# Kernel tuning notes

Hardware: AMD Instinct MI355X
Metric: run time of the kernel (lower is better)

## Reference

```python
import jax, jax.numpy as jnp
import numpy as np

N = 50000      # nodes
E = 600000     # edges
D_IN = 5
D_H = 128
EPS = 1e-5     # BatchNorm1d default eps


def batch_norm(x, gamma, beta):
    # training-mode BN over the node dimension (biased variance)
    m = jnp.mean(x, axis=0)
    v = jnp.var(x, axis=0)
    return (x - m) * jax.lax.rsqrt(v + EPS) * gamma + beta


def gcn_conv(x, W, b, src, dst, w):
    # PyG GCNConv: linear transform, add self-loops (weight 1),
    # symmetric normalization D^-1/2 A D^-1/2, scatter-add to dst, + bias.
    x = x @ W                                   # [N, out]
    n = x.shape[0]
    loop = jnp.arange(n)
    src = jnp.concatenate([src, loop])
    dst = jnp.concatenate([dst, loop])
    w = jnp.concatenate([w, jnp.ones((n,), w.dtype)])
    deg = jax.ops.segment_sum(w, dst, num_segments=n)
    dis = jnp.where(deg > 0, jax.lax.rsqrt(jnp.maximum(deg, 1e-12)), 0.0)
    norm = dis[src] * w * dis[dst]              # [E+N]
    msgs = norm[:, None] * x[src]               # gather + scale
    return jax.ops.segment_sum(msgs, dst, num_segments=n) + b


def setup_inputs() -> dict:
    key = jax.random.key(0)
    ks = jax.random.split(key, 20)
    s_in = 1.0 / np.sqrt(D_IN)
    s_h = 1.0 / np.sqrt(D_H)
    return {
        "h": jax.random.normal(ks[0], (N, D_IN), jnp.float32),
        "edge_index": jax.random.randint(ks[1], (2, E), 0, N),
        "edge_weight": jax.random.uniform(ks[2], (E,), jnp.float32),
        "g0": 1.0 + 0.1 * jax.random.normal(ks[3], (D_IN,), jnp.float32),
        "be0": 0.1 * jax.random.normal(ks[4], (D_IN,), jnp.float32),
        "W1": jax.random.normal(ks[5], (D_IN, D_H), jnp.float32) * s_in,
        "b1": jax.random.normal(ks[6], (D_H,), jnp.float32) * s_in,
        "g1": 1.0 + 0.1 * jax.random.normal(ks[7], (D_H,), jnp.float32),
        "be1": 0.1 * jax.random.normal(ks[8], (D_H,), jnp.float32),
        "W2": jax.random.normal(ks[9], (D_H, D_H), jnp.float32) * s_h,
        "b2": jax.random.normal(ks[10], (D_H,), jnp.float32) * s_h,
        "g2": 1.0 + 0.1 * jax.random.normal(ks[11], (D_H,), jnp.float32),
        "be2": 0.1 * jax.random.normal(ks[12], (D_H,), jnp.float32),
        "Wmu": jax.random.normal(ks[13], (D_H, D_H), jnp.float32) * s_h,
        "bmu": jax.random.normal(ks[14], (D_H,), jnp.float32) * s_h,
        "Wls": jax.random.normal(ks[15], (D_H, D_H), jnp.float32) * s_h,
        "bls": jax.random.normal(ks[16], (D_H,), jnp.float32) * s_h,
    }


def reference(h, edge_index, edge_weight, g0, be0, W1, b1, g1, be1,
              W2, b2, g2, be2, Wmu, bmu, Wls, bls):
    src, dst = edge_index[0], edge_index[1]
    h = batch_norm(h, g0, be0)
    h = jax.nn.relu(batch_norm(gcn_conv(h, W1, b1, src, dst, edge_weight), g1, be1))
    # dropout p=0.1 treated as eval-mode (identity)
    h = jax.nn.relu(batch_norm(gcn_conv(h, W2, b2, src, dst, edge_weight), g2, be2))
    mu = h @ Wmu + bmu
    log_std = h @ Wls + bls
    return (mu, log_std)
```

## Files before the change

kernel.cpp:

```cpp
#include <hip/hip_runtime.h>

#define N_NODES 50000
#define N_EDGES 600000
#define D_IN 5
#define D_H 128
#define BN_EPS 1e-5f
#define SCAN_BLOCKS ((N_NODES + 255) / 256)
#define FIX_SCALE 16777216.0f
#define FIX_INV   (1.0f / 16777216.0f)

typedef __bf16 bf16x8 __attribute__((ext_vector_type(8)));
typedef float  f32x4  __attribute__((ext_vector_type(4)));

__device__ inline unsigned short f2bfb(float f) {
    unsigned u = __builtin_bit_cast(unsigned, f);
    unsigned r = u + 0x7fffu + ((u >> 16) & 1u);
    return (unsigned short)(r >> 16);
}
__device__ inline float bflo(unsigned u) { return __builtin_bit_cast(float, u << 16); }
__device__ inline float bfhi(unsigned u) { return __builtin_bit_cast(float, u & 0xffff0000u); }

__device__ inline void stage_b(const unsigned short* __restrict__ Bt,
                               uint4* __restrict__ lds, int t)
{
#pragma unroll
    for (int i = 0; i < 8; ++i) {
        int slot = i * 256 + t;
        int fid = slot >> 6;
        int l = slot & 63;
        int row = (fid >> 2) * 16 + (l & 15);
        int boff = ((l >> 4) * 16 + (fid & 3) * 64) >> 1;
        lds[slot] = *(const uint4*)(Bt + row * D_H + boff);
    }
}

__global__ __launch_bounds__(256) void k_wprep(const float* __restrict__ W2,
                                               const float* __restrict__ Wmu,
                                               const float* __restrict__ Wls,
                                               unsigned short* __restrict__ T2,
                                               unsigned short* __restrict__ Tmu,
                                               unsigned short* __restrict__ Tls)
{
    int mat = blockIdx.x >> 6;
    int idx = (blockIdx.x & 63) * 256 + threadIdx.x;
    const float* W = (mat == 0) ? W2 : (mat == 1) ? Wmu : Wls;
    unsigned short* T = (mat == 0) ? T2 : (mat == 1) ? Tmu : Tls;
    int k = idx >> 7, n = idx & 127;
    T[n * D_H + k] = f2bfb(W[idx]);
}

__global__ __launch_bounds__(256) void k_bn0_stats(const float* __restrict__ h,
                                                   float* __restrict__ stats)
{
    __shared__ float ss[D_IN], sq[D_IN];
    int t = threadIdx.x;
    if (t < D_IN) { ss[t] = 0.f; sq[t] = 0.f; }
    __syncthreads();
    int node = blockIdx.x * blockDim.x + t;
    float v[D_IN];
#pragma unroll
    for (int f = 0; f < D_IN; ++f)
        v[f] = (node < N_NODES) ? h[node * D_IN + f] : 0.f;
    int lane = t & 63;
#pragma unroll
    for (int f = 0; f < D_IN; ++f) {
        float s = v[f], q = v[f] * v[f];
        for (int off = 32; off > 0; off >>= 1) {
            s += __shfl_down(s, off);
            q += __shfl_down(q, off);
        }
        if (lane == 0) { atomicAdd(&ss[f], s); atomicAdd(&sq[f], q); }
    }
    __syncthreads();
    if (t < D_IN) {
        atomicAdd(&stats[t], ss[t]);
        atomicAdd(&stats[D_IN + t], sq[t]);
    }
}

__global__ __launch_bounds__(256) void k_deg_count(const int* __restrict__ dst,
                                                   const float* __restrict__ w,
                                                   unsigned long long* __restrict__ degcnt)
{
    int e = blockIdx.x * blockDim.x + threadIdx.x;
    if (e < N_EDGES) {
        int d = dst[e];
        unsigned long long fx = (unsigned long long)(w[e] * FIX_SCALE + 0.5f);
        atomicAdd(degcnt + d, (1ull << 40) | fx);
    }
}

__global__ __launch_bounds__(256) void k_scan1(const unsigned long long* __restrict__ degcnt,
                                               float* __restrict__ dis,
                                               int* __restrict__ blocksums)
{
    __shared__ int sm[256];
    int t = threadIdx.x;
    int i = blockIdx.x * 256 + t;
    int c = 0;
    if (i < N_NODES) {
        unsigned long long v = degcnt[i];
        c = (int)(v >> 40);
        float deg = (float)(v & ((1ull << 40) - 1)) * FIX_INV;
        dis[i] = rsqrtf(deg + 1.0f);
    }
    sm[t] = c;
    __syncthreads();
    for (int off = 128; off > 0; off >>= 1) {
        if (t < off) sm[t] += sm[t + off];
        __syncthreads();
    }
    if (t == 0) blocksums[blockIdx.x] = sm[0];
}

__global__ __launch_bounds__(256) void k_scan2(int* __restrict__ blocksums,
                                               int* __restrict__ rowptr)
{
    __shared__ int sm[256];
    int t = threadIdx.x;
    int c = (t < SCAN_BLOCKS) ? blocksums[t] : 0;
    sm[t] = c;
    __syncthreads();
    for (int off = 1; off < 256; off <<= 1) {
        int v = (t >= off) ? sm[t - off] : 0;
        __syncthreads();
        sm[t] += v;
        __syncthreads();
    }
    if (t < SCAN_BLOCKS) blocksums[t] = sm[t] - c;
    if (t == 255) rowptr[N_NODES] = sm[255];
}

__global__ __launch_bounds__(256) void k_scan3(const unsigned long long* __restrict__ degcnt,
                                               int* __restrict__ rowptr,
                                               int* __restrict__ cursor,
                                               const int* __restrict__ blocksums)
{
    __shared__ int sm[256];
    int t = threadIdx.x;
    int i = blockIdx.x * 256 + t;
    int c = (i < N_NODES) ? (int)(degcnt[i] >> 40) : 0;
    sm[t] = c;
    __syncthreads();
    for (int off = 1; off < 256; off <<= 1) {
        int v = (t >= off) ? sm[t - off] : 0;
        __syncthreads();
        sm[t] += v;
        __syncthreads();
    }
    if (i < N_NODES) {
        int pos = blocksums[blockIdx.x] + sm[t] - c;
        rowptr[i] = pos;
        cursor[i] = pos;
    }
}

__global__ __launch_bounds__(256) void k_fill(const int* __restrict__ src,
                                              const int* __restrict__ dst,
                                              const float* __restrict__ w,
                                              const float* __restrict__ dis,
                                              int* __restrict__ cursor,
                                              int2* __restrict__ csr)
{
    int e = blockIdx.x * blockDim.x + threadIdx.x;
    if (e < N_EDGES) {
        int s = src[e], d = dst[e];
        float nm = dis[s] * w[e] * dis[d];
        int pos = atomicAdd(cursor + d, 1);
        int2 pk;
        pk.x = s;
        pk.y = __builtin_bit_cast(int, nm);
        csr[pos] = pk;
    }
}

__global__ __launch_bounds__(256) void k_agg0(const float* __restrict__ h,
                                              const float* __restrict__ stats,
                                              const float* __restrict__ g0,
                                              const float* __restrict__ be0,
                                              const int* __restrict__ rowptr,
                                              const int2* __restrict__ csr,
                                              const float* __restrict__ dis,
                                              float* __restrict__ agg)
{
    int n = blockIdx.x * blockDim.x + threadIdx.x;
    if (n >= N_NODES) return;
    float sc[D_IN], sh[D_IN];
#pragma unroll
    for (int f = 0; f < D_IN; ++f) {
        float m = stats[f] * (1.0f / N_NODES);
        float var = stats[D_IN + f] * (1.0f / N_NODES) - m * m;
        sc[f] = rsqrtf(var + BN_EPS) * g0[f];
        sh[f] = be0[f] - m * sc[f];
    }
    float dn = dis[n];
    float sl = dn * dn;
    float acc[D_IN];
#pragma unroll
    for (int f = 0; f < D_IN; ++f)
        acc[f] = sl * (h[n * D_IN + f] * sc[f] + sh[f]);
    int e0 = rowptr[n], e1 = rowptr[n + 1];
    for (int e = e0; e < e1; ++e) {
        int2 pk = csr[e];
        int s = pk.x;
        float nm = __builtin_bit_cast(float, pk.y);
#pragma unroll
        for (int f = 0; f < D_IN; ++f)
            acc[f] += nm * (h[s * D_IN + f] * sc[f] + sh[f]);
    }
#pragma unroll
    for (int f = 0; f < D_IN; ++f)
        agg[n * D_IN + f] = acc[f];
}

__global__ __launch_bounds__(256) void k_l1(const float* __restrict__ agg,
                                            const float* __restrict__ W1,
                                            const float* __restrict__ b1,
                                            float* __restrict__ x,
                                            float* __restrict__ stats)
{
    __shared__ float sm_s[256], sm_q[256];
    int t = threadIdx.x;
    int idx0 = blockIdx.x * 256 + t;
    int f = idx0 & (D_H - 1);
    float w[D_IN];
#pragma unroll
    for (int k = 0; k < D_IN; ++k) w[k] = W1[k * D_H + f];
    float b = b1[f];
    float s = 0.f, q = 0.f;
    const int stride = 512 * 256;
    for (int idx = idx0; idx < N_NODES * D_H; idx += stride) {
        int n = idx >> 7;
        const float* a = agg + n * D_IN;
        float v = b;
#pragma unroll
        for (int k = 0; k < D_IN; ++k) v += w[k] * a[k];
        x[idx] = v;
        s += v;
        q += v * v;
    }
    sm_s[t] = s;
    sm_q[t] = q;
    __syncthreads();
    if (t < D_H) {
        atomicAdd(stats + t, sm_s[t] + sm_s[t + D_H]);
        atomicAdd(stats + D_H + t, sm_q[t] + sm_q[t + D_H]);
    }
}

__global__ __launch_bounds__(256) void k_bn_relu_f32_bf16(const float* __restrict__ x,
                                                          const float* __restrict__ stats,
                                                          const float* __restrict__ g,
                                                          const float* __restrict__ be,
                                                          unsigned short* __restrict__ y)
{
    int i4 = blockIdx.x * blockDim.x + threadIdx.x;
    if (i4 >= N_NODES * D_H / 4) return;
    int f0 = (i4 & 31) * 4;
    float4 s4 = *(const float4*)(stats + f0);
    float4 q4 = *(const float4*)(stats + D_H + f0);
    float4 g4 = *(const float4*)(g + f0);
    float4 b4 = *(const float4*)(be + f0);
    float4 v = *(const float4*)(x + (size_t)i4 * 4);
    const float inv = 1.0f / N_NODES;
    float m, var, sc, sh;
    float r0, r1, r2, r3;
    m = s4.x * inv; var = q4.x * inv - m * m; sc = rsqrtf(var + BN_EPS) * g4.x; sh = b4.x - m * sc;
    r0 = fmaxf(v.x * sc + sh, 0.f);
    m = s4.y * inv; var = q4.y * inv - m * m; sc = rsqrtf(var + BN_EPS) * g4.y; sh = b4.y - m * sc;
    r1 = fmaxf(v.y * sc + sh, 0.f);
    m = s4.z * inv; var = q4.z * inv - m * m; sc = rsqrtf(var + BN_EPS) * g4.z; sh = b4.z - m * sc;
    r2 = fmaxf(v.z * sc + sh, 0.f);
    m = s4.w * inv; var = q4.w * inv - m * m; sc = rsqrtf(var + BN_EPS) * g4.w; sh = b4.w - m * sc;
    r3 = fmaxf(v.w * sc + sh, 0.f);
    uint2 o;
    o.x = (unsigned)f2bfb(r0) | ((unsigned)f2bfb(r1) << 16);
    o.y = (unsigned)f2bfb(r2) | ((unsigned)f2bfb(r3) << 16);
    *(uint2*)(y + (size_t)i4 * 4) = o;
}

__global__ __launch_bounds__(256) void k_bn_relu_bf16_bf16(const unsigned short* __restrict__ x,
                                                           const float* __restrict__ stats,
                                                           const float* __restrict__ g,
                                                           const float* __restrict__ be,
                                                           unsigned short* __restrict__ y)
{
    int i4 = blockIdx.x * blockDim.x + threadIdx.x;
    if (i4 >= N_NODES * D_H / 4) return;
    int f0 = (i4 & 31) * 4;
    float4 s4 = *(const float4*)(stats + f0);
    float4 q4 = *(const float4*)(stats + D_H + f0);
    float4 g4 = *(const float4*)(g + f0);
    float4 b4 = *(const float4*)(be + f0);
    uint2 iv = *(const uint2*)(x + (size_t)i4 * 4);
    const float inv = 1.0f / N_NODES;
    float m, var, sc, sh;
    float r0, r1, r2, r3;
    m = s4.x * inv; var = q4.x * inv - m * m; sc = rsqrtf(var + BN_EPS) * g4.x; sh = b4.x - m * sc;
    r0 = fmaxf(bflo(iv.x) * sc + sh, 0.f);
    m = s4.y * inv; var = q4.y * inv - m * m; sc = rsqrtf(var + BN_EPS) * g4.y; sh = b4.y - m * sc;
    r1 = fmaxf(bfhi(iv.x) * sc + sh, 0.f);
    m = s4.z * inv; var = q4.z * inv - m * m; sc = rsqrtf(var + BN_EPS) * g4.z; sh = b4.z - m * sc;
    r2 = fmaxf(bflo(iv.y) * sc + sh, 0.f);
    m = s4.w * inv; var = q4.w * inv - m * m; sc = rsqrtf(var + BN_EPS) * g4.w; sh = b4.w - m * sc;
    r3 = fmaxf(bfhi(iv.y) * sc + sh, 0.f);
    uint2 o;
    o.x = (unsigned)f2bfb(r0) | ((unsigned)f2bfb(r1) << 16);
    o.y = (unsigned)f2bfb(r2) | ((unsigned)f2bfb(r3) << 16);
    *(uint2*)(y + (size_t)i4 * 4) = o;
}

__global__ __launch_bounds__(256) void k_agg128(const unsigned short* __restrict__ h,
                                                const int* __restrict__ rowptr,
                                                const int2* __restrict__ csr,
                                                const float* __restrict__ dis,
                                                unsigned short* __restrict__ outb)
{
    int t = threadIdx.x;
    int n = blockIdx.x * 16 + (t >> 4);
    int f0 = (t & 15) * 8;
    if (n >= N_NODES) return;
    float d = dis[n];
    float sl = d * d;
    uint4 hv = *(const uint4*)(h + (size_t)n * D_H + f0);
    float a0 = sl * bflo(hv.x), a1 = sl * bfhi(hv.x);
    float a2 = sl * bflo(hv.y), a3 = sl * bfhi(hv.y);
    float a4 = sl * bflo(hv.z), a5 = sl * bfhi(hv.z);
    float a6 = sl * bflo(hv.w), a7 = sl * bfhi(hv.w);
    int e = rowptr[n], e1 = rowptr[n + 1];
    for (; e + 4 <= e1; e += 4) {
        int2 p0 = csr[e + 0], p1 = csr[e + 1], p2 = csr[e + 2], p3 = csr[e + 3];
        float w0 = __builtin_bit_cast(float, p0.y);
        float w1 = __builtin_bit_cast(float, p1.y);
        float w2 = __builtin_bit_cast(float, p2.y);
        float w3 = __builtin_bit_cast(float, p3.y);
        uint4 v0 = *(const uint4*)(h + (size_t)p0.x * D_H + f0);
        uint4 v1 = *(const uint4*)(h + (size_t)p1.x * D_H + f0);
        uint4 v2 = *(const uint4*)(h + (size_t)p2.x * D_H + f0);
        uint4 v3 = *(const uint4*)(h + (size_t)p3.x * D_H + f0);
        a0 += w0 * bflo(v0.x) + w1 * bflo(v1.x) + w2 * bflo(v2.x) + w3 * bflo(v3.x);
        a1 += w0 * bfhi(v0.x) + w1 * bfhi(v1.x) + w2 * bfhi(v2.x) + w3 * bfhi(v3.x);
        a2 += w0 * bflo(v0.y) + w1 * bflo(v1.y) + w2 * bflo(v2.y) + w3 * bflo(v3.y);
        a3 += w0 * bfhi(v0.y) + w1 * bfhi(v1.y) + w2 * bfhi(v2.y) + w3 * bfhi(v3.y);
        a4 += w0 * bflo(v0.z) + w1 * bflo(v1.z) + w2 * bflo(v2.z) + w3 * bflo(v3.z);
        a5 += w0 * bfhi(v0.z) + w1 * bfhi(v1.z) + w2 * bfhi(v2.z) + w3 * bfhi(v3.z);
        a6 += w0 * bflo(v0.w) + w1 * bflo(v1.w) + w2 * bflo(v2.w) + w3 * bflo(v3.w);
        a7 += w0 * bfhi(v0.w) + w1 * bfhi(v1.w) + w2 * bfhi(v2.w) + w3 * bfhi(v3.w);
    }
    for (; e < e1; ++e) {
        int2 pk = csr[e];
        float nm = __builtin_bit_cast(float, pk.y);
        uint4 v = *(const uint4*)(h + (size_t)pk.x * D_H + f0);
        a0 += nm * bflo(v.x); a1 += nm * bfhi(v.x);
        a2 += nm * bflo(v.y); a3 += nm * bfhi(v.y);
        a4 += nm * bflo(v.z); a5 += nm * bfhi(v.z);
        a6 += nm * bflo(v.w); a7 += nm * bfhi(v.w);
    }
    uint4 o;
    o.x = (unsigned)f2bfb(a0) | ((unsigned)f2bfb(a1) << 16);
    o.y = (unsigned)f2bfb(a2) | ((unsigned)f2bfb(a3) << 16);
    o.z = (unsigned)f2bfb(a4) | ((unsigned)f2bfb(a5) << 16);
    o.w = (unsigned)f2bfb(a6) | ((unsigned)f2bfb(a7) << 16);
    *(uint4*)(outb + (size_t)n * D_H + f0) = o;
}

__global__ __launch_bounds__(256) void k_gemm_mf(const unsigned short* __restrict__ A,
                                                 const unsigned short* __restrict__ Bt,
                                                 const float* __restrict__ bias,
                                                 unsigned short* __restrict__ C,
                                                 float* __restrict__ stats)
{
    __shared__ uint4 ldsB[2048];
    __shared__ float sm_s[D_H], sm_q[D_H];
    int t = threadIdx.x;
    if (t < D_H) { sm_s[t] = 0.f; sm_q[t] = 0.f; }
    stage_b(Bt, ldsB, t);
    int wave = t >> 6, lane = t & 63;
    int m = lane & 15, quad = lane >> 4;
    int r0 = blockIdx.x * 64 + wave * 16;
    int arow = r0 + m < N_NODES ? r0 + m : N_NODES - 1;
    const bf16x8* ap = (const bf16x8*)(A + (size_t)arow * D_H + quad * 8);
    bf16x8 af[4];
#pragma unroll
    for (int ks = 0; ks < 4; ++ks) af[ks] = ap[ks * 4];
    __syncthreads();
    const bf16x8* bf = (const bf16x8*)ldsB;
    f32x4 acc[8];
#pragma unroll
    for (int ct = 0; ct < 8; ++ct) acc[ct] = (f32x4)(0.f);
#pragma unroll
    for (int ks = 0; ks < 4; ++ks) {
#pragma unroll
        for (int ct = 0; ct < 8; ++ct) {
            acc[ct] = __builtin_amdgcn_mfma_f32_16x16x32_bf16(
                af[ks], bf[(ct * 4 + ks) * 64 + lane], acc[ct], 0, 0, 0);
        }
    }
#pragma unroll
    for (int ct = 0; ct < 8; ++ct) {
        int col = ct * 16 + m;
        float bv = bias[col];
        float s = 0.f, q = 0.f;
#pragma unroll
        for (int r = 0; r < 4; ++r) {
            int rr = r0 + quad * 4 + r;
            if (rr < N_NODES) {
                float v = acc[ct][r] + bv;
                C[(size_t)rr * D_H + col] = f2bfb(v);
                s += v; q += v * v;
            }
        }
        atomicAdd(&sm_s[col], s);
        atomicAdd(&sm_q[col], q);
    }
    __syncthreads();
    if (t < D_H) {
        atomicAdd(stats + t, sm_s[t]);
        atomicAdd(stats + D_H + t, sm_q[t]);
    }
}

__global__ __launch_bounds__(256) void k_gemm_out_mf(const unsigned short* __restrict__ A,
                                                     const unsigned short* __restrict__ Btmu,
                                                     const float* __restrict__ bmu,
                                                     const unsigned short* __restrict__ Btls,
                                                     const float* __restrict__ bls,
                                                     float* __restrict__ out)
{
    __shared__ uint4 ldsB[2048];
    int t = threadIdx.x;
    int wave = t >> 6, lane = t & 63;
    int m = lane & 15, quad = lane >> 4;
    int r0 = blockIdx.x * 64 + wave * 16;
    int arow = r0 + m < N_NODES ? r0 + m : N_NODES - 1;
    const bf16x8* ap = (const bf16x8*)(A + (size_t)arow * D_H + quad * 8);
    bf16x8 af[4];
#pragma unroll
    for (int ks = 0; ks < 4; ++ks) af[ks] = ap[ks * 4];
    const bf16x8* bf = (const bf16x8*)ldsB;
#pragma unroll
    for (int half = 0; half < 2; ++half) {
        if (half) __syncthreads();
        stage_b(half ? Btls : Btmu, ldsB, t);
        __syncthreads();
        const float* bias = half ? bls : bmu;
        float* C = out + (half ? (size_t)N_NODES * D_H : 0);
        f32x4 acc[8];
#pragma unroll
        for (int ct = 0; ct < 8; ++ct) acc[ct] = (f32x4)(0.f);
#pragma unroll
        for (int ks = 0; ks < 4; ++ks) {
#pragma unroll
            for (int ct = 0; ct < 8; ++ct) {
                acc[ct] = __builtin_amdgcn_mfma_f32_16x16x32_bf16(
                    af[ks], bf[(ct * 4 + ks) * 64 + lane], acc[ct], 0, 0, 0);
            }
        }
#pragma unroll
        for (int ct = 0; ct < 8; ++ct) {
            int col = ct * 16 + m;
            float bv = bias[col];
#pragma unroll
            for (int r = 0; r < 4; ++r) {
                int rr = r0 + quad * 4 + r;
                if (rr < N_NODES)
                    C[(size_t)rr * D_H + col] = acc[ct][r] + bv;
            }
        }
    }
}

extern "C" void kernel_launch(void* const* d_in, const int* in_sizes, int n_in,
                              void* d_out, int out_size, void* d_ws, size_t ws_size,
                              hipStream_t stream)
{
    const float* h   = (const float*)d_in[0];
    const int*   eidx = (const int*)d_in[1];
    const float* ew  = (const float*)d_in[2];
    const float* g0  = (const float*)d_in[3];
    const float* be0 = (const float*)d_in[4];
    const float* W1  = (const float*)d_in[5];
    const float* b1  = (const float*)d_in[6];
    const float* g1  = (const float*)d_in[7];
    const float* be1 = (const float*)d_in[8];
    const float* W2  = (const float*)d_in[9];
    const float* b2  = (const float*)d_in[10];
    const float* g2  = (const float*)d_in[11];
    const float* be2 = (const float*)d_in[12];
    const float* Wmu = (const float*)d_in[13];
    const float* bmu = (const float*)d_in[14];
    const float* Wls = (const float*)d_in[15];
    const float* bls = (const float*)d_in[16];
    const int* srcv = eidx;
    const int* dstv = eidx + N_EDGES;
    float* out = (float*)d_out;

    char* ws = (char*)d_ws;
    size_t off = 0;
    auto alloc = [&](size_t bytes) -> char* {
        char* p = ws + off;
        off += (bytes + 255) & ~(size_t)255;
        return p;
    };
    float* stats0  = (float*)alloc(16 * 4);
    float* stats1  = (float*)alloc(256 * 4);
    float* stats2  = (float*)alloc(256 * 4);
    unsigned long long* degcnt = (unsigned long long*)alloc(N_NODES * 8);
    size_t zero_bytes = off;
    int*   rowptr  = (int*)  alloc((N_NODES + 1) * 4);
    float* dis     = (float*)alloc(N_NODES * 4);
    int*   cursor  = (int*)  alloc(N_NODES * 4);
    int*   blocksums = (int*)alloc(256 * 4);
    int2*  csr     = (int2*) alloc((size_t)N_EDGES * 8);
    float* agg0    = (float*)alloc(N_NODES * D_IN * 4);
    float* bufA    = (float*)alloc((size_t)N_NODES * D_H * 4);
    unsigned short* bufAh = (unsigned short*)alloc((size_t)N_NODES * D_H * 2);
    unsigned short* bufBh = (unsigned short*)alloc((size_t)N_NODES * D_H * 2);
    unsigned short* Wt2   = (unsigned short*)alloc(D_H * D_H * 2);
    unsigned short* Wtmu  = (unsigned short*)alloc(D_H * D_H * 2);
    unsigned short* Wtls  = (unsigned short*)alloc(D_H * D_H * 2);
    (void)ws_size; (void)in_sizes; (void)n_in; (void)out_size;

    hipMemsetAsync(d_ws, 0, zero_bytes, stream);

    k_wprep<<<192, 256, 0, stream>>>(W2, Wmu, Wls, Wt2, Wtmu, Wtls);
    k_bn0_stats<<<(N_NODES + 255) / 256, 256, 0, stream>>>(h, stats0);
    k_deg_count<<<(N_EDGES + 255) / 256, 256, 0, stream>>>(dstv, ew, degcnt);
    k_scan1<<<SCAN_BLOCKS, 256, 0, stream>>>(degcnt, dis, blocksums);
    k_scan2<<<1, 256, 0, stream>>>(blocksums, rowptr);
    k_scan3<<<SCAN_BLOCKS, 256, 0, stream>>>(degcnt, rowptr, cursor, blocksums);
    k_fill<<<(N_EDGES + 255) / 256, 256, 0, stream>>>(srcv, dstv, ew, dis, cursor, csr);
    k_agg0<<<(N_NODES + 255) / 256, 256, 0, stream>>>(h, stats0, g0, be0, rowptr,
                                                      csr, dis, agg0);
    k_l1<<<512, 256, 0, stream>>>(agg0, W1, b1, bufA, stats1);
    k_bn_relu_f32_bf16<<<(N_NODES * D_H / 4 + 255) / 256, 256, 0, stream>>>(bufA, stats1, g1, be1, bufAh);
    k_agg128<<<(N_NODES + 15) / 16, 256, 0, stream>>>(bufAh, rowptr, csr, dis, bufBh);
    k_gemm_mf<<<(N_NODES + 63) / 64, 256, 0, stream>>>(bufBh, Wt2, b2, bufAh, stats2);
    k_bn_relu_bf16_bf16<<<(N_NODES * D_H / 4 + 255) / 256, 256, 0, stream>>>(bufAh, stats2, g2, be2, bufBh);
    k_gemm_out_mf<<<(N_NODES + 63) / 64, 256, 0, stream>>>(bufBh, Wtmu, bmu, Wtls, bls, out);
}
```

Measured before the change: 325.7 us.

## Fuse BN+ReLU into gather and GEMM loads, merge prep kernels, rank-based CSR fill

Merges the weight-transpose, BN0-stats and degree-count kernels into one launch. The degree atomic's return value now records each edge's rank, so the CSR fill computes positions without a second atomic cursor. The standalone BN+ReLU passes are removed: layer-1 output is written directly as bf16, and BN+ReLU is applied on the fly when the aggregation reads gathered neighbours and when the output GEMM loads its A operand. The destination-side normalisation is factored out and applied once per node. This cuts kernel launches and full-size intermediate round trips, at the cost of recomputing BN+ReLU for every gathered neighbour and an extra rank array.

```diff
diff --git a/kernel.cpp b/kernel.cpp
--- a/kernel.cpp
+++ b/kernel.cpp
@@ -6,6 +6,7 @@
 #define D_H 128
 #define BN_EPS 1e-5f
 #define SCAN_BLOCKS ((N_NODES + 255) / 256)
+#define DEG_BLOCKS ((N_EDGES + 255) / 256)
 #define FIX_SCALE 16777216.0f
 #define FIX_INV   (1.0f / 16777216.0f)
 
@@ -34,59 +35,60 @@
     }
 }
 
-__global__ __launch_bounds__(256) void k_wprep(const float* __restrict__ W2,
-                                               const float* __restrict__ Wmu,
-                                               const float* __restrict__ Wls,
-                                               unsigned short* __restrict__ T2,
-                                               unsigned short* __restrict__ Tmu,
-                                               unsigned short* __restrict__ Tls)
-{
-    int mat = blockIdx.x >> 6;
-    int idx = (blockIdx.x & 63) * 256 + threadIdx.x;
-    const float* W = (mat == 0) ? W2 : (mat == 1) ? Wmu : Wls;
-    unsigned short* T = (mat == 0) ? T2 : (mat == 1) ? Tmu : Tls;
-    int k = idx >> 7, n = idx & 127;
-    T[n * D_H + k] = f2bfb(W[idx]);
-}
-
-__global__ __launch_bounds__(256) void k_bn0_stats(const float* __restrict__ h,
-                                                   float* __restrict__ stats)
+__global__ __launch_bounds__(256) void k_prep(const float* __restrict__ W2,
+                                              const float* __restrict__ Wmu,
+                                              const float* __restrict__ Wls,
+                                              unsigned short* __restrict__ T2,
+                                              unsigned short* __restrict__ Tmu,
+                                              unsigned short* __restrict__ Tls,
+                                              const float* __restrict__ h,
+                                              float* __restrict__ stats0,
+                                              const int* __restrict__ dst,
+                                              const float* __restrict__ w,
+                                              unsigned long long* __restrict__ degcnt,
+                                              int* __restrict__ rank)
 {
     __shared__ float ss[D_IN], sq[D_IN];
-    int t = threadIdx.x;
-    if (t < D_IN) { ss[t] = 0.f; sq[t] = 0.f; }
-    __syncthreads();
-    int node = blockIdx.x * blockDim.x + t;
-    float v[D_IN];
-#pragma unroll
-    for (int f = 0; f < D_IN; ++f)
-        v[f] = (node < N_NODES) ? h[node * D_IN + f] : 0.f;
-    int lane = t & 63;
-#pragma unroll
-    for (int f = 0; f < D_IN; ++f) {
-        float s = v[f], q = v[f] * v[f];
-        for (int off = 32; off > 0; off >>= 1) {
-            s += __shfl_down(s, off);
-            q += __shfl_down(q, off);
-        }
-        if (lane == 0) { atomicAdd(&ss[f], s); atomicAdd(&sq[f], q); }
-    }
-    __syncthreads();
-    if (t < D_IN) {
-        atomicAdd(&stats[t], ss[t]);
-        atomicAdd(&stats[D_IN + t], sq[t]);
-    }
-}
-
-__global__ __launch_bounds__(256) void k_deg_count(const int* __restrict__ dst,
-                                                   const float* __restrict__ w,
-                                                   unsigned long long* __restrict__ degcnt)
-{
-    int e = blockIdx.x * blockDim.x + threadIdx.x;
-    if (e < N_EDGES) {
-        int d = dst[e];
-        unsigned long long fx = (unsigned long long)(w[e] * FIX_SCALE + 0.5f);
-        atomicAdd(degcnt + d, (1ull << 40) | fx);
+    int b = blockIdx.x;
+    int t = threadIdx.x;
+    if (b < 192) {
+        int mat = b >> 6;
+        int idx = (b & 63) * 256 + t;
+        const float* W = (mat == 0) ? W2 : (mat == 1) ? Wmu : Wls;
+        unsigned short* T = (mat == 0) ? T2 : (mat == 1) ? Tmu : Tls;
+        int k = idx >> 7, n = idx & 127;
+        T[n * D_H + k] = f2bfb(W[idx]);
+    } else if (b < 192 + SCAN_BLOCKS) {
+        if (t < D_IN) { ss[t] = 0.f; sq[t] = 0.f; }
+        __syncthreads();
+        int node = (b - 192) * 256 + t;
+        float v[D_IN];
+#pragma unroll
+        for (int f = 0; f < D_IN; ++f)
+            v[f] = (node < N_NODES) ? h[node * D_IN + f] : 0.f;
+        int lane = t & 63;
+#pragma unroll
+        for (int f = 0; f < D_IN; ++f) {
+            float s = v[f], q = v[f] * v[f];
+            for (int off = 32; off > 0; off >>= 1) {
+                s += __shfl_down(s, off);
+                q += __shfl_down(q, off);
+            }
+            if (lane == 0) { atomicAdd(&ss[f], s); atomicAdd(&sq[f], q); }
+        }
+        __syncthreads();
+        if (t < D_IN) {
+            atomicAdd(&stats0[t], ss[t]);
+            atomicAdd(&stats0[D_IN + t], sq[t]);
+        }
+    } else {
+        int e = (b - 192 - SCAN_BLOCKS) * 256 + t;
+        if (e < N_EDGES) {
+            int d = dst[e];
+            unsigned long long fx = (unsigned long long)(w[e] * FIX_SCALE + 0.5f);
+            unsigned long long old = atomicAdd(degcnt + d, (1ull << 40) | fx);
+            rank[e] = (int)(old >> 40);
+        }
     }
 }
 
@@ -133,7 +135,6 @@
 
 __global__ __launch_bounds__(256) void k_scan3(const unsigned long long* __restrict__ degcnt,
                                                int* __restrict__ rowptr,
-                                               int* __restrict__ cursor,
                                                const int* __restrict__ blocksums)
 {
     __shared__ int sm[256];
@@ -148,28 +149,26 @@
         sm[t] += v;
         __syncthreads();
     }
-    if (i < N_NODES) {
-        int pos = blocksums[blockIdx.x] + sm[t] - c;
-        rowptr[i] = pos;
-        cursor[i] = pos;
-    }
+    if (i < N_NODES)
+        rowptr[i] = blocksums[blockIdx.x] + sm[t] - c;
 }
 
 __global__ __launch_bounds__(256) void k_fill(const int* __restrict__ src,
                                               const int* __restrict__ dst,
                                               const float* __restrict__ w,
                                               const float* __restrict__ dis,
-                                              int* __restrict__ cursor,
+                                              const int* __restrict__ rowptr,
+                                              const int* __restrict__ rank,
                                               int2* __restrict__ csr)
 {
     int e = blockIdx.x * blockDim.x + threadIdx.x;
     if (e < N_EDGES) {
         int s = src[e], d = dst[e];
-        float nm = dis[s] * w[e] * dis[d];
-        int pos = atomicAdd(cursor + d, 1);
+        float pn = dis[s] * w[e];
+        int pos = rowptr[d] + rank[e];
         int2 pk;
         pk.x = s;
-        pk.y = __builtin_bit_cast(int, nm);
+        pk.y = __builtin_bit_cast(int, pn);
         csr[pos] = pk;
     }
 }
@@ -194,123 +193,67 @@
         sh[f] = be0[f] - m * sc[f];
     }
     float dn = dis[n];
-    float sl = dn * dn;
     float acc[D_IN];
 #pragma unroll
     for (int f = 0; f < D_IN; ++f)
-        acc[f] = sl * (h[n * D_IN + f] * sc[f] + sh[f]);
+        acc[f] = dn * (h[n * D_IN + f] * sc[f] + sh[f]);
     int e0 = rowptr[n], e1 = rowptr[n + 1];
     for (int e = e0; e < e1; ++e) {
         int2 pk = csr[e];
         int s = pk.x;
-        float nm = __builtin_bit_cast(float, pk.y);
+        float pn = __builtin_bit_cast(float, pk.y);
 #pragma unroll
         for (int f = 0; f < D_IN; ++f)
-            acc[f] += nm * (h[s * D_IN + f] * sc[f] + sh[f]);
+            acc[f] += pn * (h[s * D_IN + f] * sc[f] + sh[f]);
     }
 #pragma unroll
     for (int f = 0; f < D_IN; ++f)
-        agg[n * D_IN + f] = acc[f];
+        agg[n * D_IN + f] = dn * acc[f];
 }
 
 __global__ __launch_bounds__(256) void k_l1(const float* __restrict__ agg,
                                             const float* __restrict__ W1,
                                             const float* __restrict__ b1,
-                                            float* __restrict__ x,
+                                            unsigned short* __restrict__ x,
                                             float* __restrict__ stats)
 {
-    __shared__ float sm_s[256], sm_q[256];
-    int t = threadIdx.x;
+    __shared__ float sm_s[D_H], sm_q[D_H];
+    int t = threadIdx.x;
+    if (t < D_H) { sm_s[t] = 0.f; sm_q[t] = 0.f; }
+    __syncthreads();
     int idx0 = blockIdx.x * 256 + t;
-    int f = idx0 & (D_H - 1);
-    float w[D_IN];
-#pragma unroll
-    for (int k = 0; k < D_IN; ++k) w[k] = W1[k * D_H + f];
-    float b = b1[f];
-    float s = 0.f, q = 0.f;
+    int f0 = (idx0 & 63) * 2;
+    float wa[D_IN], wb[D_IN];
+#pragma unroll
+    for (int k = 0; k < D_IN; ++k) {
+        wa[k] = W1[k * D_H + f0];
+        wb[k] = W1[k * D_H + f0 + 1];
+    }
+    float ba = b1[f0], bb = b1[f0 + 1];
+    float s0 = 0.f, q0 = 0.f, s1 = 0.f, q1 = 0.f;
     const int stride = 512 * 256;
-    for (int idx = idx0; idx < N_NODES * D_H; idx += stride) {
-        int n = idx >> 7;
+    for (int idx = idx0; idx < N_NODES * 64; idx += stride) {
+        int n = idx >> 6;
         const float* a = agg + n * D_IN;
-        float v = b;
-#pragma unroll
-        for (int k = 0; k < D_IN; ++k) v += w[k] * a[k];
-        x[idx] = v;
-        s += v;
-        q += v * v;
-    }
-    sm_s[t] = s;
-    sm_q[t] = q;
+        float v0 = ba, v1 = bb;
+#pragma unroll
+        for (int k = 0; k < D_IN; ++k) { v0 += wa[k] * a[k]; v1 += wb[k] * a[k]; }
+        ((unsigned*)x)[idx] = (unsigned)f2bfb(v0) | ((unsigned)f2bfb(v1) << 16);
+        s0 += v0; q0 += v0 * v0; s1 += v1; q1 += v1 * v1;
+    }
+    atomicAdd(&sm_s[f0], s0); atomicAdd(&sm_s[f0 + 1], s1);
+    atomicAdd(&sm_q[f0], q0); atomicAdd(&sm_q[f0 + 1], q1);
     __syncthreads();
     if (t < D_H) {
-        atomicAdd(stats + t, sm_s[t] + sm_s[t + D_H]);
-        atomicAdd(stats + D_H + t, sm_q[t] + sm_q[t + D_H]);
-    }
-}
-
-__global__ __launch_bounds__(256) void k_bn_relu_f32_bf16(const float* __restrict__ x,
-                                                          const float* __restrict__ stats,
-                                                          const float* __restrict__ g,
-                                                          const float* __restrict__ be,
-                                                          unsigned short* __restrict__ y)
-{
-    int i4 = blockIdx.x * blockDim.x + threadIdx.x;
-    if (i4 >= N_NODES * D_H / 4) return;
-    int f0 = (i4 & 31) * 4;
-    float4 s4 = *(const float4*)(stats + f0);
-    float4 q4 = *(const float4*)(stats + D_H + f0);
-    float4 g4 = *(const float4*)(g + f0);
-    float4 b4 = *(const float4*)(be + f0);
-    float4 v = *(const float4*)(x + (size_t)i4 * 4);
-    const float inv = 1.0f / N_NODES;
-    float m, var, sc, sh;
-    float r0, r1, r2, r3;
-    m = s4.x * inv; var = q4.x * inv - m * m; sc = rsqrtf(var + BN_EPS) * g4.x; sh = b4.x - m * sc;
-    r0 = fmaxf(v.x * sc + sh, 0.f);
-    m = s4.y * inv; var = q4.y * inv - m * m; sc = rsqrtf(var + BN_EPS) * g4.y; sh = b4.y - m * sc;
-    r1 = fmaxf(v.y * sc + sh, 0.f);
-    m = s4.z * inv; var = q4.z * inv - m * m; sc = rsqrtf(var + BN_EPS) * g4.z; sh = b4.z - m * sc;
-    r2 = fmaxf(v.z * sc + sh, 0.f);
-    m = s4.w * inv; var = q4.w * inv - m * m; sc = rsqrtf(var + BN_EPS) * g4.w; sh = b4.w - m * sc;
-    r3 = fmaxf(v.w * sc + sh, 0.f);
-    uint2 o;
-    o.x = (unsigned)f2bfb(r0) | ((unsigned)f2bfb(r1) << 16);
-    o.y = (unsigned)f2bfb(r2) | ((unsigned)f2bfb(r3) << 16);
-    *(uint2*)(y + (size_t)i4 * 4) = o;
-}
-
-__global__ __launch_bounds__(256) void k_bn_relu_bf16_bf16(const unsigned short* __restrict__ x,
-                                                           const float* __restrict__ stats,
-                                                           const float* __restrict__ g,
-                                                           const float* __restrict__ be,
-                                                           unsigned short* __restrict__ y)
-{
-    int i4 = blockIdx.x * blockDim.x + threadIdx.x;
-    if (i4 >= N_NODES * D_H / 4) return;
-    int f0 = (i4 & 31) * 4;
-    float4 s4 = *(const float4*)(stats + f0);
-    float4 q4 = *(const float4*)(stats + D_H + f0);
-    float4 g4 = *(const float4*)(g + f0);
-    float4 b4 = *(const float4*)(be + f0);
-    uint2 iv = *(const uint2*)(x + (size_t)i4 * 4);
-    const float inv = 1.0f / N_NODES;
-    float m, var, sc, sh;
-    float r0, r1, r2, r3;
-    m = s4.x * inv; var = q4.x * inv - m * m; sc = rsqrtf(var + BN_EPS) * g4.x; sh = b4.x - m * sc;
-    r0 = fmaxf(bflo(iv.x) * sc + sh, 0.f);
-    m = s4.y * inv; var = q4.y * inv - m * m; sc = rsqrtf(var + BN_EPS) * g4.y; sh = b4.y - m * sc;
-    r1 = fmaxf(bfhi(iv.x) * sc + sh, 0.f);
-    m = s4.z * inv; var = q4.z * inv - m * m; sc = rsqrtf(var + BN_EPS) * g4.z; sh = b4.z - m * sc;
-    r2 = fmaxf(bflo(iv.y) * sc + sh, 0.f);
-    m = s4.w * inv; var = q4.w * inv - m * m; sc = rsqrtf(var + BN_EPS) * g4.w; sh = b4.w - m * sc;
-    r3 = fmaxf(bfhi(iv.y) * sc + sh, 0.f);
-    uint2 o;
-    o.x = (unsigned)f2bfb(r0) | ((unsigned)f2bfb(r1) << 16);
-    o.y = (unsigned)f2bfb(r2) | ((unsigned)f2bfb(r3) << 16);
-    *(uint2*)(y + (size_t)i4 * 4) = o;
-}
-
-__global__ __launch_bounds__(256) void k_agg128(const unsigned short* __restrict__ h,
+        atomicAdd(stats + t, sm_s[t]);
+        atomicAdd(stats + D_H + t, sm_q[t]);
+    }
+}
+
+__global__ __launch_bounds__(256) void k_agg128(const unsigned short* __restrict__ x,
+                                                const float* __restrict__ stats,
+                                                const float* __restrict__ g,
+                                                const float* __restrict__ be,
                                                 const int* __restrict__ rowptr,
                                                 const int2* __restrict__ csr,
                                                 const float* __restrict__ dis,
@@ -320,13 +263,22 @@
     int n = blockIdx.x * 16 + (t >> 4);
     int f0 = (t & 15) * 8;
     if (n >= N_NODES) return;
-    float d = dis[n];
-    float sl = d * d;
-    uint4 hv = *(const uint4*)(h + (size_t)n * D_H + f0);
-    float a0 = sl * bflo(hv.x), a1 = sl * bfhi(hv.x);
-    float a2 = sl * bflo(hv.y), a3 = sl * bfhi(hv.y);
-    float a4 = sl * bflo(hv.z), a5 = sl * bfhi(hv.z);
-    float a6 = sl * bflo(hv.w), a7 = sl * bfhi(hv.w);
+    float sc[8], sh[8];
+    const float inv = 1.0f / N_NODES;
+#pragma unroll
+    for (int j = 0; j < 8; ++j) {
+        float m = stats[f0 + j] * inv;
+        float var = stats[D_H + f0 + j] * inv - m * m;
+        sc[j] = rsqrtf(var + BN_EPS) * g[f0 + j];
+        sh[j] = be[f0 + j] - m * sc[j];
+    }
+#define BNR(val, j) fmaxf((val) * sc[j] + sh[j], 0.f)
+    float dn = dis[n];
+    uint4 hv = *(const uint4*)(x + (size_t)n * D_H + f0);
+    float a0 = dn * BNR(bflo(hv.x), 0), a1 = dn * BNR(bfhi(hv.x), 1);
+    float a2 = dn * BNR(bflo(hv.y), 2), a3 = dn * BNR(bfhi(hv.y), 3);
+    float a4 = dn * BNR(bflo(hv.z), 4), a5 = dn * BNR(bfhi(hv.z), 5);
+    float a6 = dn * BNR(bflo(hv.w), 6), a7 = dn * BNR(bfhi(hv.w), 7);
     int e = rowptr[n], e1 = rowptr[n + 1];
     for (; e + 4 <= e1; e += 4) {
         int2 p0 = csr[e + 0], p1 = csr[e + 1], p2 = csr[e + 2], p3 = csr[e + 3];
@@ -334,33 +286,34 @@
         float w1 = __builtin_bit_cast(float, p1.y);
         float w2 = __builtin_bit_cast(float, p2.y);
         float w3 = __builtin_bit_cast(float, p3.y);
-        uint4 v0 = *(const uint4*)(h + (size_t)p0.x * D_H + f0);
-        uint4 v1 = *(const uint4*)(h + (size_t)p1.x * D_H + f0);
-        uint4 v2 = *(const uint4*)(h + (size_t)p2.x * D_H + f0);
-        uint4 v3 = *(const uint4*)(h + (size_t)p3.x * D_H + f0);
-        a0 += w0 * bflo(v0.x) + w1 * bflo(v1.x) + w2 * bflo(v2.x) + w3 * bflo(v3.x);
-        a1 += w0 * bfhi(v0.x) + w1 * bfhi(v1.x) + w2 * bfhi(v2.x) + w3 * bfhi(v3.x);
-        a2 += w0 * bflo(v0.y) + w1 * bflo(v1.y) + w2 * bflo(v2.y) + w3 * bflo(v3.y);
-        a3 += w0 * bfhi(v0.y) + w1 * bfhi(v1.y) + w2 * bfhi(v2.y) + w3 * bfhi(v3.y);
-        a4 += w0 * bflo(v0.z) + w1 * bflo(v1.z) + w2 * bflo(v2.z) + w3 * bflo(v3.z);
-        a5 += w0 * bfhi(v0.z) + w1 * bfhi(v1.z) + w2 * bfhi(v2.z) + w3 * bfhi(v3.z);
-        a6 += w0 * bflo(v0.w) + w1 * bflo(v1.w) + w2 * bflo(v2.w) + w3 * bflo(v3.w);
-        a7 += w0 * bfhi(v0.w) + w1 * bfhi(v1.w) + w2 * bfhi(v2.w) + w3 * bfhi(v3.w);
+        uint4 v0 = *(const uint4*)(x + (size_t)p0.x * D_H + f0);
+        uint4 v1 = *(const uint4*)(x + (size_t)p1.x * D_H + f0);
+        uint4 v2 = *(const uint4*)(x + (size_t)p2.x * D_H + f0);
+        uint4 v3 = *(const uint4*)(x + (size_t)p3.x * D_H + f0);
+        a0 += w0 * BNR(bflo(v0.x), 0) + w1 * BNR(bflo(v1.x), 0) + w2 * BNR(bflo(v2.x), 0) + w3 * BNR(bflo(v3.x), 0);
+        a1 += w0 * BNR(bfhi(v0.x), 1) + w1 * BNR(bfhi(v1.x), 1) + w2 * BNR(bfhi(v2.x), 1) + w3 * BNR(bfhi(v3.x), 1);
+        a2 += w0 * BNR(bflo(v0.y), 2) + w1 * BNR(bflo(v1.y), 2) + w2 * BNR(bflo(v2.y), 2) + w3 * BNR(bflo(v3.y), 2);
+        a3 += w0 * BNR(bfhi(v0.y), 3) + w1 * BNR(bfhi(v1.y), 3) + w2 * BNR(bfhi(v2.y), 3) + w3 * BNR(bfhi(v3.y), 3);
+        a4 += w0 * BNR(bflo(v0.z), 4) + w1 * BNR(bflo(v1.z), 4) + w2 * BNR(bflo(v2.z), 4) + w3 * BNR(bflo(v3.z), 4);
+        a5 += w0 * BNR(bfhi(v0.z), 5) + w1 * BNR(bfhi(v1.z), 5) + w2 * BNR(bfhi(v2.z), 5) + w3 * BNR(bfhi(v3.z), 5);
+        a6 += w0 * BNR(bflo(v0.w), 6) + w1 * BNR(bflo(v1.w), 6) + w2 * BNR(bflo(v2.w), 6) + w3 * BNR(bflo(v3.w), 6);
+        a7 += w0 * BNR(bfhi(v0.w), 7) + w1 * BNR(bfhi(v1.w), 7) + w2 * BNR(bfhi(v2.w), 7) + w3 * BNR(bfhi(v3.w), 7);
     }
     for (; e < e1; ++e) {
         int2 pk = csr[e];
-        float nm = __builtin_bit_cast(float, pk.y);
-        uint4 v = *(const uint4*)(h + (size_t)pk.x * D_H + f0);
-        a0 += nm * bflo(v.x); a1 += nm * bfhi(v.x);
-        a2 += nm * bflo(v.y); a3 += nm * bfhi(v.y);
-        a4 += nm * bflo(v.z); a5 += nm * bfhi(v.z);
-        a6 += nm * bflo(v.w); a7 += nm * bfhi(v.w);
-    }
+        float pn = __builtin_bit_cast(float, pk.y);
+        uint4 v = *(const uint4*)(x + (size_t)pk.x * D_H + f0);
+        a0 += pn * BNR(bflo(v.x), 0); a1 += pn * BNR(bfhi(v.x), 1);
+        a2 += pn * BNR(bflo(v.y), 2); a3 += pn * BNR(bfhi(v.y), 3);
+        a4 += pn * BNR(bflo(v.z), 4); a5 += pn * BNR(bfhi(v.z), 5);
+        a6 += pn * BNR(bflo(v.w), 6); a7 += pn * BNR(bfhi(v.w), 7);
+    }
+#undef BNR
     uint4 o;
-    o.x = (unsigned)f2bfb(a0) | ((unsigned)f2bfb(a1) << 16);
-    o.y = (unsigned)f2bfb(a2) | ((unsigned)f2bfb(a3) << 16);
-    o.z = (unsigned)f2bfb(a4) | ((unsigned)f2bfb(a5) << 16);
-    o.w = (unsigned)f2bfb(a6) | ((unsigned)f2bfb(a7) << 16);
+    o.x = (unsigned)f2bfb(dn * a0) | ((unsigned)f2bfb(dn * a1) << 16);
+    o.y = (unsigned)f2bfb(dn * a2) | ((unsigned)f2bfb(dn * a3) << 16);
+    o.z = (unsigned)f2bfb(dn * a4) | ((unsigned)f2bfb(dn * a5) << 16);
+    o.w = (unsigned)f2bfb(dn * a6) | ((unsigned)f2bfb(dn * a7) << 16);
     *(uint4*)(outb + (size_t)n * D_H + f0) = o;
 }
 
@@ -421,6 +374,9 @@
 }
 
 __global__ __launch_bounds__(256) void k_gemm_out_mf(const unsigned short* __restrict__ A,
+                                                     const float* __restrict__ stats,
+                                                     const float* __restrict__ g,
+                                                     const float* __restrict__ be,
                                                      const unsigned short* __restrict__ Btmu,
                                                      const float* __restrict__ bmu,
                                                      const unsigned short* __restrict__ Btls,
@@ -433,10 +389,32 @@
     int m = lane & 15, quad = lane >> 4;
     int r0 = blockIdx.x * 64 + wave * 16;
     int arow = r0 + m < N_NODES ? r0 + m : N_NODES - 1;
-    const bf16x8* ap = (const bf16x8*)(A + (size_t)arow * D_H + quad * 8);
+    const unsigned short* arowp = A + (size_t)arow * D_H + quad * 8;
+    const float inv = 1.0f / N_NODES;
     bf16x8 af[4];
 #pragma unroll
-    for (int ks = 0; ks < 4; ++ks) af[ks] = ap[ks * 4];
+    for (int ks = 0; ks < 4; ++ks) {
+        uint4 av = *(const uint4*)(arowp + ks * 32);
+        float vals[8] = { bflo(av.x), bfhi(av.x), bflo(av.y), bfhi(av.y),
+                          bflo(av.z), bfhi(av.z), bflo(av.w), bfhi(av.w) };
+        int fb = quad * 8 + ks * 32;
+        unsigned short o[8];
+#pragma unroll
+        for (int j = 0; j < 8; ++j) {
+            int f = fb + j;
+            float mm = stats[f] * inv;
+            float var = stats[D_H + f] * inv - mm * mm;
+            float scv = rsqrtf(var + BN_EPS) * g[f];
+            float shv = be[f] - mm * scv;
+            o[j] = f2bfb(fmaxf(vals[j] * scv + shv, 0.f));
+        }
+        uint4 pk;
+        pk.x = (unsigned)o[0] | ((unsigned)o[1] << 16);
+        pk.y = (unsigned)o[2] | ((unsigned)o[3] << 16);
+        pk.z = (unsigned)o[4] | ((unsigned)o[5] << 16);
+        pk.w = (unsigned)o[6] | ((unsigned)o[7] << 16);
+        af[ks] = __builtin_bit_cast(bf16x8, pk);
+    }
     const bf16x8* bf = (const bf16x8*)ldsB;
 #pragma unroll
     for (int half = 0; half < 2; ++half) {
@@ -509,13 +487,13 @@
     size_t zero_bytes = off;
     int*   rowptr  = (int*)  alloc((N_NODES + 1) * 4);
     float* dis     = (float*)alloc(N_NODES * 4);
-    int*   cursor  = (int*)  alloc(N_NODES * 4);
+    int*   rank    = (int*)  alloc((size_t)N_EDGES * 4);
     int*   blocksums = (int*)alloc(256 * 4);
     int2*  csr     = (int2*) alloc((size_t)N_EDGES * 8);
     float* agg0    = (float*)alloc(N_NODES * D_IN * 4);
-    float* bufA    = (float*)alloc((size_t)N_NODES * D_H * 4);
-    unsigned short* bufAh = (unsigned short*)alloc((size_t)N_NODES * D_H * 2);
-    unsigned short* bufBh = (unsigned short*)alloc((size_t)N_NODES * D_H * 2);
+    unsigned short* x1h  = (unsigned short*)alloc((size_t)N_NODES * D_H * 2);
+    unsigned short* aggh = (unsigned short*)alloc((size_t)N_NODES * D_H * 2);
+    unsigned short* c2h  = (unsigned short*)alloc((size_t)N_NODES * D_H * 2);
     unsigned short* Wt2   = (unsigned short*)alloc(D_H * D_H * 2);
     unsigned short* Wtmu  = (unsigned short*)alloc(D_H * D_H * 2);
     unsigned short* Wtls  = (unsigned short*)alloc(D_H * D_H * 2);
@@ -523,19 +501,17 @@
 
     hipMemsetAsync(d_ws, 0, zero_bytes, stream);
 
-    k_wprep<<<192, 256, 0, stream>>>(W2, Wmu, Wls, Wt2, Wtmu, Wtls);
-    k_bn0_stats<<<(N_NODES + 255) / 256, 256, 0, stream>>>(h, stats0);
-    k_deg_count<<<(N_EDGES + 255) / 256, 256, 0, stream>>>(dstv, ew, degcnt);
+    k_prep<<<192 + SCAN_BLOCKS + DEG_BLOCKS, 256, 0, stream>>>(
+        W2, Wmu, Wls, Wt2, Wtmu, Wtls, h, stats0, dstv, ew, degcnt, rank);
     k_scan1<<<SCAN_BLOCKS, 256, 0, stream>>>(degcnt, dis, blocksums);
     k_scan2<<<1, 256, 0, stream>>>(blocksums, rowptr);
-    k_scan3<<<SCAN_BLOCKS, 256, 0, stream>>>(degcnt, rowptr, cursor, blocksums);
-    k_fill<<<(N_EDGES + 255) / 256, 256, 0, stream>>>(srcv, dstv, ew, dis, cursor, csr);
-    k_agg0<<<(N_NODES + 255) / 256, 256, 0, stream>>>(h, stats0, g0, be0, rowptr,
-                                                      csr, dis, agg0);
-    k_l1<<<512, 256, 0, stream>>>(agg0, W1, b1, bufA, stats1);
-    k_bn_relu_f32_bf16<<<(N_NODES * D_H / 4 + 255) / 256, 256, 0, stream>>>(bufA, stats1, g1, be1, bufAh);
-    k_agg128<<<(N_NODES + 15) / 16, 256, 0, stream>>>(bufAh, rowptr, csr, dis, bufBh);
-    k_gemm_mf<<<(N_NODES + 63) / 64, 256, 0, stream>>>(bufBh, Wt2, b2, bufAh, stats2);
-    k_bn_relu_bf16_bf16<<<(N_NODES * D_H / 4 + 255) / 256, 256, 0, stream>>>(bufAh, stats2, g2, be2, bufBh);
-    k_gemm_out_mf<<<(N_NODES + 63) / 64, 256, 0, stream>>>(bufBh, Wtmu, bmu, Wtls, bls, out);
-}
+    k_scan3<<<SCAN_BLOCKS, 256, 0, stream>>>(degcnt, rowptr, blocksums);
+    k_fill<<<DEG_BLOCKS, 256, 0, stream>>>(srcv, dstv, ew, dis, rowptr, rank, csr);
+    k_agg0<<<SCAN_BLOCKS, 256, 0, stream>>>(h, stats0, g0, be0, rowptr, csr, dis, agg0);
+    k_l1<<<512, 256, 0, stream>>>(agg0, W1, b1, x1h, stats1);
+    k_agg128<<<(N_NODES + 15) / 16, 256, 0, stream>>>(x1h, stats1, g1, be1,
+                                                      rowptr, csr, dis, aggh);
+    k_gemm_mf<<<(N_NODES + 63) / 64, 256, 0, stream>>>(aggh, Wt2, b2, c2h, stats2);
+    k_gemm_out_mf<<<(N_NODES + 63) / 64, 256, 0, stream>>>(c2h, stats2, g2, be2,
+                                                           Wtmu, bmu, Wtls, bls, out);
+}
```

Result: faster. 281.5 us (-13.6%).
